# Performance work log

Hardware: AMD Instinct MI355X
Metric: run time of the kernel (lower is better)

Reference implementation:

```python
import math
import jax, jax.numpy as jnp
import numpy as np

jax.config.update("jax_enable_x64", True)

P_PRIME = 1000003            # prime modulus; p-1 = 2*3*166667
N_FACTORS = (2, 3, 166667)   # prime factors of p-1 (for primitive-root search)
B, NPATCH, L, K, DIM = 4, 784, 9, 16, 28  # batch, patches/sample, patch len, kernels, map dim


def _modpow(base, exp, p, nbits=21):
    """Vectorized modular exponentiation (square-and-multiply), int64, exponents < 2^nbits."""
    shape = jnp.broadcast_shapes(jnp.shape(base), jnp.shape(exp))
    b0 = jnp.broadcast_to(jnp.asarray(base, jnp.int64) % p, shape)
    e = jnp.broadcast_to(jnp.asarray(exp, jnp.int64), shape)
    def body(i, c):
        res, b = c
        res = jnp.where(((e >> i) & 1) == 1, (res * b) % p, res)
        return (res, (b * b) % p)
    res, _ = jax.lax.fori_loop(0, nbits, body, (jnp.ones(shape, jnp.int64), b0))
    return res


def _decrypt_ips(ct0, cts, y, sk_y, g, p):
    """IPFE decrypt + BSGS discrete log. ct0:[B,P] cts:[B,P,L] y:[K,L] sk_y:[K] -> signed ip [K,B,P]."""
    n = p - 1
    powed = _modpow(cts[None], jnp.mod(y, n)[:, None, None, :], p)   # [K,B,P,L]
    num = powed[..., 0]
    for i in range(1, L):                                            # fixed small L=9
        num = (num * powed[..., i]) % p
    denom = _modpow(ct0[None], jnp.mod(sk_y, n)[:, None, None], p)   # [K,B,P]
    val = (num * _modpow(denom, p - 2, p)) % p                       # = g^{<x,y>} mod p (Fermat inverse)
    # baby-step giant-step over group order n
    m = math.isqrt(n - 1) + 1
    n_giant = -(-n // m)
    baby = _modpow(jnp.int64(g), jnp.arange(m, dtype=jnp.int64), p)  # g^j, j in [0,m)
    order = jnp.argsort(baby)
    sb = baby[order]
    ginv_m = _modpow(jnp.int64(g), jnp.int64((n - m) % n), p)        # g^{-m}
    pt = _modpow(ginv_m, jnp.arange(n_giant, dtype=jnp.int64), p)    # g^{-m*i}
    gamma = (val.reshape(-1)[:, None] * pt[None, :]) % p             # [T, n_giant] giant steps
    pos = jnp.clip(jnp.searchsorted(sb, gamma), 0, m - 1)
    hit = sb[pos] == gamma
    cand = jnp.arange(n_giant, dtype=jnp.int64)[None, :] * m + order[pos]
    ip = jnp.min(jnp.where(hit, cand, n), axis=1)                    # unique match: ip = i*m + j
    ip = jnp.where(ip > n // 2, ip - n, ip)                          # signed representative
    return ip.reshape(K, ct0.shape[0], ct0.shape[1])


def _bn(x, g_, b_, m_, v_):
    s = g_ * jax.lax.rsqrt(v_ + 1e-5)
    return (x - m_[None, :, None, None]) * s[None, :, None, None] + b_[None, :, None, None]


def _conv(x, w, b):
    o = jax.lax.conv_general_dilated(x, w, (1, 1), ((1, 1), (1, 1)),
                                     dimension_numbers=("NCHW", "OIHW", "NCHW"))
    return o + b[None, :, None, None]


def _pool(x):
    return jax.lax.reduce_window(x, jnp.array(-jnp.inf, x.dtype), jax.lax.max,
                                 (1, 1, 2, 2), (1, 1, 2, 2), "VALID")


def _forward(ct0, cts, y, sk_y, bias1, bn1_g, bn1_b, bn1_m, bn1_v,
             conv2_w, conv2_b, bn2_g, bn2_b, bn2_m, bn2_v,
             conv3_w, conv3_b, bn3_g, bn3_b, bn3_m, bn3_v,
             fc1_w, fc1_b, fc2_w, fc2_b, g, p):
    ip = _decrypt_ips(ct0, cts, y, sk_y, g, p)                       # [K,B,P] int64
    maps = ip.astype(jnp.float32) / 10000.0 + bias1[:, None, None]   # dequantize + conv1 bias
    feat = jnp.transpose(maps, (1, 0, 2)).reshape(-1, K, DIM, DIM)   # [B,16,28,28]
    feat = _pool(jax.nn.relu(_bn(feat, bn1_g, bn1_b, bn1_m, bn1_v)))
    feat = _pool(jax.nn.relu(_bn(_conv(feat, conv2_w, conv2_b), bn2_g, bn2_b, bn2_m, bn2_v)))
    feat = _pool(jax.nn.relu(_bn(_conv(feat, conv3_w, conv3_b), bn3_g, bn3_b, bn3_m, bn3_v)))
    flat = feat.reshape(feat.shape[0], -1)                           # [B,576]
    h = jax.nn.relu(flat @ fc1_w.T + fc1_b)                          # dropout = identity (eval mode)
    return h @ fc2_w.T + fc2_b                                       # [B,10]


def setup_inputs():
    rng = np.random.default_rng(0)
    p, n = P_PRIME, P_PRIME - 1
    assert all(p % d for d in range(2, math.isqrt(p) + 1))           # p prime
    g = next(gg for gg in range(2, 200)
             if all(pow(gg, n // q, p) != 1 for q in N_FACTORS))      # primitive root mod p
    s = rng.integers(1, n, size=L)                                    # master secret
    pk = [pow(g, int(si), p) for si in s]
    y = rng.integers(-50, 51, size=(K, L)).astype(np.int64)          # round(w*10000)
    x = rng.integers(0, 21, size=(B, NPATCH, L))                     # quantized patch values
    r = rng.integers(1, n, size=(B, NPATCH))
    gx = [pow(g, t, p) for t in range(21)]
    ct0 = np.zeros((B, NPATCH), dtype=np.int64)
    cts = np.zeros((B, NPATCH, L), dtype=np.int64)
    for b in range(B):
        for j in range(NPATCH):
            rr = int(r[b, j])
            ct0[b, j] = pow(g, rr, p)
            for i in range(L):
                cts[b, j, i] = pow(pk[i], rr, p) * gx[x[b, j, i]] % p
    sk_y = np.array([sum(int(s[i]) * int(y[k, i]) for i in range(L)) % n
                     for k in range(K)], dtype=np.int64)
    f32 = lambda a: jnp.asarray(a, jnp.float32)
    def rn(*sh):
        return f32(rng.standard_normal(sh) * 0.1)
    def bnp(c):
        return (f32(1.0 + 0.1 * rng.standard_normal(c)), rn(c), rn(c), f32(rng.random(c) + 0.5))
    bn1_g, bn1_b, bn1_m, bn1_v = bnp(16)
    bn2_g, bn2_b, bn2_m, bn2_v = bnp(32)
    bn3_g, bn3_b, bn3_m, bn3_v = bnp(64)
    return dict(ct0=jnp.asarray(ct0), cts=jnp.asarray(cts),
                y=jnp.asarray(y), sk_y=jnp.asarray(sk_y), bias1=rn(K),
                bn1_g=bn1_g, bn1_b=bn1_b, bn1_m=bn1_m, bn1_v=bn1_v,
                conv2_w=rn(32, 16, 3, 3), conv2_b=rn(32),
                bn2_g=bn2_g, bn2_b=bn2_b, bn2_m=bn2_m, bn2_v=bn2_v,
                conv3_w=rn(64, 32, 3, 3), conv3_b=rn(64),
                bn3_g=bn3_g, bn3_b=bn3_b, bn3_m=bn3_m, bn3_v=bn3_v,
                fc1_w=rn(128, 576), fc1_b=rn(128),
                fc2_w=rn(10, 128), fc2_b=rn(10), g=g, p=p)


def reference(ct0, cts, y, sk_y, bias1, bn1_g, bn1_b, bn1_m, bn1_v,
              conv2_w, conv2_b, bn2_g, bn2_b, bn2_m, bn2_v,
              conv3_w, conv3_b, bn3_g, bn3_b, bn3_m, bn3_v,
              fc1_w, fc1_b, fc2_w, fc2_b, g, p):
    return _forward(ct0, cts, y, sk_y, bias1, bn1_g, bn1_b, bn1_m, bn1_v,
                    conv2_w, conv2_b, bn2_g, bn2_b, bn2_m, bn2_v,
                    conv3_w, conv3_b, bn3_g, bn3_b, bn3_m, bn3_v,
                    fc1_w, fc1_b, fc2_w, fc2_b, g, p)
```

## Files before the change

### kernel.cpp

```cpp
#include <hip/hip_runtime.h>
#include <stdint.h>

#define PRIME 1000003u
#define NORD  1000002u
#define KCH   16
#define BATCH 4
#define NPATCH 784
#define LLEN  9
#define IPMAX 9000
#define TBLN  (2*IPMAX+1)
#define NBLK  128
#define ABLK  64
#define TPB   832

#define CTR_OFF   2000064
#define POOL_OFF  2001024
#define S2G_OFF   2051200
#define S3G_OFF   2076288
#define HG_OFF    2085504

__device__ __forceinline__ uint32_t mmul(uint32_t a, uint32_t b) {
    uint64_t t = (uint64_t)a * (uint64_t)b;
    uint32_t q = (uint32_t)((t * 2199016ull) >> 41);
    uint32_t r = (uint32_t)t - q * PRIME;
    return (r >= PRIME) ? r - PRIME : r;
}

__device__ __forceinline__ uint32_t mpow(uint32_t base, uint32_t exp) {
    uint32_t r = 1u, b = base;
    while (exp) {
        if (exp & 1u) r = mmul(r, b);
        b = mmul(b, b);
        exp >>= 1;
    }
    return r;
}

__device__ __forceinline__ void cstore(float* p, float v) {
    __hip_atomic_store(p, v, __ATOMIC_RELAXED, __HIP_MEMORY_SCOPE_AGENT);
}
__device__ __forceinline__ float cload(const float* p) {
    return __hip_atomic_load(p, __ATOMIC_RELAXED, __HIP_MEMORY_SCOPE_AGENT);
}

__device__ __forceinline__ void arrive8(unsigned* ctrs, int bid) {
    __syncthreads();
    if (threadIdx.x == 0)
        __hip_atomic_fetch_add(&ctrs[(bid & 7) * 16], 1u,
                               __ATOMIC_RELAXED, __HIP_MEMORY_SCOPE_AGENT);
}
__device__ __forceinline__ void wait8(unsigned* ctrs, unsigned target) {
    if (threadIdx.x == 0) {
        for (;;) {
            unsigned s = 0;
#pragma unroll
            for (int i = 0; i < 8; i++)
                s += __hip_atomic_load(&ctrs[i * 16],
                                       __ATOMIC_RELAXED, __HIP_MEMORY_SCOPE_AGENT);
            if (s >= target) break;
            __builtin_amdgcn_s_sleep(8);
        }
    }
    __syncthreads();
}

__global__ void build_table(const int* __restrict__ g_in, int16_t* __restrict__ table,
                            unsigned* __restrict__ ctrs) {
    int e = blockIdx.x * blockDim.x + threadIdx.x;
    if (e >= TBLN) return;
    if (e < 8)
        __hip_atomic_store(&ctrs[e * 16], 0u, __ATOMIC_RELAXED, __HIP_MEMORY_SCOPE_AGENT);
    int es = e - IPMAX;
    uint32_t exp = (es >= 0) ? (uint32_t)es : (uint32_t)(es + (int)NORD);
    table[mpow((uint32_t)g_in[0], exp)] = (int16_t)es;
}

__global__ void __launch_bounds__(TPB) fused(
    const int* __restrict__ ct0, const int* __restrict__ cts,
    const int* __restrict__ y, const int* __restrict__ sk_y,
    const float* __restrict__ bias1,
    const float* __restrict__ bn1_g, const float* __restrict__ bn1_b,
    const float* __restrict__ bn1_m, const float* __restrict__ bn1_v,
    const float* __restrict__ conv2_w, const float* __restrict__ conv2_b,
    const float* __restrict__ bn2_g, const float* __restrict__ bn2_b,
    const float* __restrict__ bn2_m, const float* __restrict__ bn2_v,
    const float* __restrict__ conv3_w, const float* __restrict__ conv3_b,
    const float* __restrict__ bn3_g, const float* __restrict__ bn3_b,
    const float* __restrict__ bn3_m, const float* __restrict__ bn3_v,
    const float* __restrict__ fc1_w, const float* __restrict__ fc1_b,
    const float* __restrict__ fc2_w, const float* __restrict__ fc2_b,
    const int16_t* __restrict__ table,
    float* __restrict__ pooled, float* __restrict__ s2g, float* __restrict__ s3g,
    float* __restrict__ hg, float* __restrict__ out, unsigned* __restrict__ ctrs) {

    __shared__ union {
        float raw[784];
        struct { float s1p[16][16][16]; float w[144]; float co[196]; } c2;
        struct { float s2p[32][9][9];  float w[4][288]; float co[4][49]; } c3;
        struct { float s3[576]; } d1;
        struct { float h[128]; } d2;
    } sm;

    const int bid = blockIdx.x;
    const int tid = threadIdx.x;

    if (bid < ABLK) {
        const int k = bid & 15, b = bid >> 4;
        const int* yrow = y + k * LLEN;
        int yv[LLEN];
#pragma unroll
        for (int i = 0; i < LLEN; i++) yv[i] = yrow[i];
        const uint32_t sk = (uint32_t)sk_y[k];
        const float sc  = bn1_g[k] * rsqrtf(bn1_v[k] + 1e-5f);
        const float shf = (bias1[k] - bn1_m[k]) * sc + bn1_b[k];

        if (tid < NPATCH) {
            const int j = tid;
            const int* crow = cts + ((b * NPATCH) + j) * LLEN;
            uint32_t c[LLEN];
#pragma unroll
            for (int i = 0; i < LLEN; i++) c[i] = (uint32_t)crow[i];

            uint32_t accp = 1u, accn = 1u;
#pragma unroll
            for (int bit = 5; bit >= 0; bit--) {
                accp = mmul(accp, accp);
                accn = mmul(accn, accn);
#pragma unroll
                for (int i = 0; i < LLEN; i++) {
                    int yi = yv[i];
                    int ay = (yi > 0) ? yi : -yi;
                    if ((ay >> bit) & 1) {
                        if (yi > 0) accp = mmul(accp, c[i]);
                        else        accn = mmul(accn, c[i]);
                    }
                }
            }

            uint32_t den = mpow((uint32_t)ct0[b * NPATCH + j], sk);
            den = mmul(den, accn);
            uint32_t val = mmul(accp, mpow(den, PRIME - 2u));

            int ip = (int)table[val];
            float v_ = fmaf((float)ip, sc * 1e-4f, shf);
            sm.raw[j] = fmaxf(v_, 0.0f);
        }
        __syncthreads();
        if (tid < 196) {
            int py = tid / 14, px = tid % 14;
            const float* r0 = &sm.raw[(2 * py) * 28 + 2 * px];
            float m = fmaxf(fmaxf(r0[0], r0[1]), fmaxf(r0[28], r0[29]));
            cstore(&pooled[((b * KCH) + k) * 196 + tid], m);
        }
        arrive8(ctrs, bid);
    }

    wait8(ctrs, ABLK);

    {
        const int b  = bid >> 5;
        const int oc = bid & 31;

        for (int i = tid; i < 16 * 16 * 16; i += TPB)
            ((float*)sm.c2.s1p)[i] = 0.0f;
        if (tid < 144) sm.c2.w[tid] = conv2_w[oc * 144 + tid];
        __syncthreads();
        for (int i = tid; i < 16 * 196; i += TPB) {
            int ic = i / 196, pos = i % 196;
            int yy = pos / 14, xx = pos % 14;
            sm.c2.s1p[ic][yy + 1][xx + 1] = cload(&pooled[((b * KCH) + ic) * 196 + pos]);
        }
        __syncthreads();

        if (tid < 196) {
            int oh = tid / 14, ow = tid % 14;
            float a0 = 0.0f, a1 = 0.0f, a2 = 0.0f;
#pragma unroll
            for (int ic = 0; ic < 16; ic++) {
                const float* wp = &sm.c2.w[ic * 9];
                const float* sp = &sm.c2.s1p[ic][oh][ow];
                a0 = fmaf(sp[0],  wp[0], fmaf(sp[1],  wp[1], fmaf(sp[2],  wp[2], a0)));
                a1 = fmaf(sp[16], wp[3], fmaf(sp[17], wp[4], fmaf(sp[18], wp[5], a1)));
                a2 = fmaf(sp[32], wp[6], fmaf(sp[33], wp[7], fmaf(sp[34], wp[8], a2)));
            }
            float sc = bn2_g[oc] * rsqrtf(bn2_v[oc] + 1e-5f);
            float shf = bn2_b[oc] - bn2_m[oc] * sc;
            sm.c2.co[tid] = fmaxf((a0 + a1 + a2 + conv2_b[oc]) * sc + shf, 0.0f);
        }
        __syncthreads();

        if (tid < 49) {
            int oh = tid / 7, ow = tid % 7;
            const float* c0 = &sm.c2.co[(2 * oh) * 14 + 2 * ow];
            cstore(&s2g[((b * 32 + oc) * 49) + tid],
                   fmaxf(fmaxf(c0[0], c0[1]), fmaxf(c0[14], c0[15])));
        }
    }

    arrive8(ctrs, bid);
    if (bid >= 64) return;
    wait8(ctrs, ABLK + NBLK);

    {
        const int b = bid >> 4, ocg = bid & 15;

        for (int i = tid; i < 32 * 81; i += TPB)
            ((float*)sm.c3.s2p)[i] = 0.0f;
        for (int i = tid; i < 4 * 288; i += TPB) {
            int w2 = i / 288, rr = i % 288;
            sm.c3.w[w2][rr] = conv3_w[(ocg * 4 + w2) * 288 + rr];
        }
        __syncthreads();
        for (int i = tid; i < 32 * 49; i += TPB) {
            int ic = i / 49, pos = i % 49;
            sm.c3.s2p[ic][pos / 7 + 1][pos % 7 + 1] = cload(&s2g[((b * 32 + ic) * 49) + pos]);
        }
        __syncthreads();

        const int wid = tid >> 6, lane = tid & 63;
        if (wid < 4 && lane < 49) {
            int oh = lane / 7, ow = lane % 7;
            float a0 = 0.0f, a1 = 0.0f, a2 = 0.0f;
#pragma unroll
            for (int ic = 0; ic < 32; ic++) {
                const float* wp = &sm.c3.w[wid][ic * 9];
                const float* sp = &sm.c3.s2p[ic][oh][ow];
                a0 = fmaf(sp[0],  wp[0], fmaf(sp[1],  wp[1], fmaf(sp[2],  wp[2], a0)));
                a1 = fmaf(sp[9],  wp[3], fmaf(sp[10], wp[4], fmaf(sp[11], wp[5], a1)));
                a2 = fmaf(sp[18], wp[6], fmaf(sp[19], wp[7], fmaf(sp[20], wp[8], a2)));
            }
            int oc = ocg * 4 + wid;
            float sc = bn3_g[oc] * rsqrtf(bn3_v[oc] + 1e-5f);
            float shf = bn3_b[oc] - bn3_m[oc] * sc;
            sm.c3.co[wid][lane] = fmaxf((a0 + a1 + a2 + conv3_b[oc]) * sc + shf, 0.0f);
        }
        __syncthreads();

        if (tid < 36) {
            int w2 = tid / 9, p = tid % 9;
            int oh = p / 3, ow = p % 3;
            const float* c0 = &sm.c3.co[w2][(2 * oh) * 7 + 2 * ow];
            cstore(&s3g[b * 576 + (ocg * 4 + w2) * 9 + p],
                   fmaxf(fmaxf(c0[0], c0[1]), fmaxf(c0[7], c0[8])));
        }
    }

    arrive8(ctrs, bid);
    wait8(ctrs, ABLK + NBLK + 64);

    {
        const int b = bid >> 4, og = bid & 15;
        for (int i = tid; i < 576; i += TPB) sm.d1.s3[i] = cload(&s3g[b * 576 + i]);
        __syncthreads();

        const int wid = tid >> 6, lane = tid & 63;
        if (wid < 8) {
            int o = og * 8 + wid;
            const float* w = fc1_w + o * 576;
            float acc = 0.0f;
#pragma unroll
            for (int jj = 0; jj < 9; jj++)
                acc = fmaf(sm.d1.s3[jj * 64 + lane], w[jj * 64 + lane], acc);
#pragma unroll
            for (int off = 32; off; off >>= 1) acc += __shfl_down(acc, off);
            if (lane == 0) cstore(&hg[b * 128 + o], fmaxf(acc + fc1_b[o], 0.0f));
        }
    }

    arrive8(ctrs, bid);
    if (bid >= BATCH) return;
    wait8(ctrs, ABLK + NBLK + 64 + 64);

    {
        const int b = bid;
        if (tid < 128) sm.d2.h[tid] = cload(&hg[b * 128 + tid]);
        __syncthreads();

        const int wid = tid >> 6, lane = tid & 63;
        if (wid < 10) {
            const float* w = fc2_w + wid * 128;
            float acc = fmaf(sm.d2.h[lane], w[lane], 0.0f);
            acc = fmaf(sm.d2.h[64 + lane], w[64 + lane], acc);
#pragma unroll
            for (int off = 32; off; off >>= 1) acc += __shfl_down(acc, off);
            if (lane == 0) out[b * 10 + wid] = acc + fc2_b[wid];
        }
    }
}

extern "C" void kernel_launch(void* const* d_in, const int* in_sizes, int n_in,
                              void* d_out, int out_size, void* d_ws, size_t ws_size,
                              hipStream_t stream) {
    const int*   ct0    = (const int*)d_in[0];
    const int*   cts    = (const int*)d_in[1];
    const int*   y      = (const int*)d_in[2];
    const int*   sk_y   = (const int*)d_in[3];
    const float* bias1  = (const float*)d_in[4];
    const float* bn1_g  = (const float*)d_in[5];
    const float* bn1_b  = (const float*)d_in[6];
    const float* bn1_m  = (const float*)d_in[7];
    const float* bn1_v  = (const float*)d_in[8];
    const float* conv2_w = (const float*)d_in[9];
    const float* conv2_b = (const float*)d_in[10];
    const float* bn2_g  = (const float*)d_in[11];
    const float* bn2_b  = (const float*)d_in[12];
    const float* bn2_m  = (const float*)d_in[13];
    const float* bn2_v  = (const float*)d_in[14];
    const float* conv3_w = (const float*)d_in[15];
    const float* conv3_b = (const float*)d_in[16];
    const float* bn3_g  = (const float*)d_in[17];
    const float* bn3_b  = (const float*)d_in[18];
    const float* bn3_m  = (const float*)d_in[19];
    const float* bn3_v  = (const float*)d_in[20];
    const float* fc1_w  = (const float*)d_in[21];
    const float* fc1_b  = (const float*)d_in[22];
    const float* fc2_w  = (const float*)d_in[23];
    const float* fc2_b  = (const float*)d_in[24];
    const int*   g_in   = (const int*)d_in[25];
    float* out = (float*)d_out;

    char* ws = (char*)d_ws;
    int16_t*  table  = (int16_t*)ws;
    unsigned* ctrs   = (unsigned*)(ws + CTR_OFF);
    float* pooled = (float*)(ws + POOL_OFF);
    float* s2g    = (float*)(ws + S2G_OFF);
    float* s3g    = (float*)(ws + S3G_OFF);
    float* hg     = (float*)(ws + HG_OFF);

    build_table<<<(TBLN + 255) / 256, 256, 0, stream>>>(g_in, table, ctrs);

    fused<<<NBLK, TPB, 0, stream>>>(
        ct0, cts, y, sk_y, bias1, bn1_g, bn1_b, bn1_m, bn1_v,
        conv2_w, conv2_b, bn2_g, bn2_b, bn2_m, bn2_v,
        conv3_w, conv3_b, bn3_g, bn3_b, bn3_m, bn3_v,
        fc1_w, fc1_b, fc2_w, fc2_b, table, pooled, s2g, s3g, hg, out, ctrs);
}
```

Measured before the change: 131.2 us.

## Split decrypt across all blocks, replace counter barriers with per-block phase flags, merge FC stages

The decrypt stage now runs on all 128 blocks, each handling half of a (batch, kernel) pair's patches, so the modular exponentiation work is spread across twice as many CUs. Conv2 now uses 32 blocks that each compute 4 output channels, and FC1 and FC2 run inside the same 4 blocks with the hidden vector kept in shared memory. This removes one grid barrier and the hg workspace. Summed atomic counters are replaced by per-block phase flags, and each waiter polls only the flags it depends on. The trade-offs are serial flag polling over up to 128 entries and less parallelism in the conv2 and FC1 stages.

```diff
diff --git a/kernel.cpp b/kernel.cpp
--- a/kernel.cpp
+++ b/kernel.cpp
@@ -10,14 +10,12 @@
 #define IPMAX 9000
 #define TBLN  (2*IPMAX+1)
 #define NBLK  128
-#define ABLK  64
 #define TPB   832
 
-#define CTR_OFF   2000064
-#define POOL_OFF  2001024
-#define S2G_OFF   2051200
-#define S3G_OFF   2076288
-#define HG_OFF    2085504
+#define FLAG_OFF  2000064
+#define POOL_OFF  2008256
+#define S2G_OFF   2058432
+#define S3G_OFF   2083520
 
 __device__ __forceinline__ uint32_t mmul(uint32_t a, uint32_t b) {
     uint64_t t = (uint64_t)a * (uint64_t)b;
@@ -43,33 +41,33 @@
     return __hip_atomic_load(p, __ATOMIC_RELAXED, __HIP_MEMORY_SCOPE_AGENT);
 }
 
-__device__ __forceinline__ void arrive8(unsigned* ctrs, int bid) {
+__device__ __forceinline__ void set_flag(unsigned* flags, int bid, unsigned phase) {
     __syncthreads();
     if (threadIdx.x == 0)
-        __hip_atomic_fetch_add(&ctrs[(bid & 7) * 16], 1u,
-                               __ATOMIC_RELAXED, __HIP_MEMORY_SCOPE_AGENT);
-}
-__device__ __forceinline__ void wait8(unsigned* ctrs, unsigned target) {
+        __hip_atomic_store(&flags[bid * 16], phase,
+                           __ATOMIC_RELAXED, __HIP_MEMORY_SCOPE_AGENT);
+}
+__device__ __forceinline__ void wait_flags(unsigned* flags, int n, unsigned phase) {
     if (threadIdx.x == 0) {
-        for (;;) {
-            unsigned s = 0;
-#pragma unroll
-            for (int i = 0; i < 8; i++)
-                s += __hip_atomic_load(&ctrs[i * 16],
-                                       __ATOMIC_RELAXED, __HIP_MEMORY_SCOPE_AGENT);
-            if (s >= target) break;
-            __builtin_amdgcn_s_sleep(8);
+        int i = 0;
+        while (i < n) {
+            if (__hip_atomic_load(&flags[i * 16],
+                                  __ATOMIC_RELAXED, __HIP_MEMORY_SCOPE_AGENT) >= phase) {
+                i++;
+            } else {
+                __builtin_amdgcn_s_sleep(8);
+            }
         }
     }
     __syncthreads();
 }
 
 __global__ void build_table(const int* __restrict__ g_in, int16_t* __restrict__ table,
-                            unsigned* __restrict__ ctrs) {
+                            unsigned* __restrict__ flags) {
     int e = blockIdx.x * blockDim.x + threadIdx.x;
     if (e >= TBLN) return;
-    if (e < 8)
-        __hip_atomic_store(&ctrs[e * 16], 0u, __ATOMIC_RELAXED, __HIP_MEMORY_SCOPE_AGENT);
+    if (e < NBLK)
+        __hip_atomic_store(&flags[e * 16], 0u, __ATOMIC_RELAXED, __HIP_MEMORY_SCOPE_AGENT);
     int es = e - IPMAX;
     uint32_t exp = (es >= 0) ? (uint32_t)es : (uint32_t)(es + (int)NORD);
     table[mpow((uint32_t)g_in[0], exp)] = (int16_t)es;
@@ -91,21 +89,21 @@
     const float* __restrict__ fc2_w, const float* __restrict__ fc2_b,
     const int16_t* __restrict__ table,
     float* __restrict__ pooled, float* __restrict__ s2g, float* __restrict__ s3g,
-    float* __restrict__ hg, float* __restrict__ out, unsigned* __restrict__ ctrs) {
+    float* __restrict__ out, unsigned* __restrict__ flags) {
 
     __shared__ union {
-        float raw[784];
-        struct { float s1p[16][16][16]; float w[144]; float co[196]; } c2;
+        float raw[392];
+        struct { float s1p[16][16][16]; float w[4][144]; float co[4][196]; } c2;
         struct { float s2p[32][9][9];  float w[4][288]; float co[4][49]; } c3;
-        struct { float s3[576]; } d1;
-        struct { float h[128]; } d2;
+        struct { float s3[576]; float h[128]; } d;
     } sm;
 
     const int bid = blockIdx.x;
     const int tid = threadIdx.x;
 
-    if (bid < ABLK) {
-        const int k = bid & 15, b = bid >> 4;
+    {
+        const int pair = bid >> 1, half = bid & 1;
+        const int k = pair & 15, b = pair >> 4;
         const int* yrow = y + k * LLEN;
         int yv[LLEN];
 #pragma unroll
@@ -114,8 +112,8 @@
         const float sc  = bn1_g[k] * rsqrtf(bn1_v[k] + 1e-5f);
         const float shf = (bias1[k] - bn1_m[k]) * sc + bn1_b[k];
 
-        if (tid < NPATCH) {
-            const int j = tid;
+        if (tid < 392) {
+            const int j = half * 392 + tid;
             const int* crow = cts + ((b * NPATCH) + j) * LLEN;
             uint32_t c[LLEN];
 #pragma unroll
@@ -143,27 +141,27 @@
 
             int ip = (int)table[val];
             float v_ = fmaf((float)ip, sc * 1e-4f, shf);
-            sm.raw[j] = fmaxf(v_, 0.0f);
-        }
-        __syncthreads();
-        if (tid < 196) {
-            int py = tid / 14, px = tid % 14;
-            const float* r0 = &sm.raw[(2 * py) * 28 + 2 * px];
+            sm.raw[tid] = fmaxf(v_, 0.0f);
+        }
+        __syncthreads();
+        if (tid < 98) {
+            int pyl = tid / 14, px = tid % 14;
+            const float* r0 = &sm.raw[(2 * pyl) * 28 + 2 * px];
             float m = fmaxf(fmaxf(r0[0], r0[1]), fmaxf(r0[28], r0[29]));
-            cstore(&pooled[((b * KCH) + k) * 196 + tid], m);
-        }
-        arrive8(ctrs, bid);
-    }
-
-    wait8(ctrs, ABLK);
-
-    {
-        const int b  = bid >> 5;
-        const int oc = bid & 31;
+            cstore(&pooled[((b * KCH) + k) * 196 + (half * 7 + pyl) * 14 + px], m);
+        }
+    }
+    set_flag(flags, bid, 1u);
+    if (bid >= 64) return;
+
+    if (bid < 32) {
+        wait_flags(flags, NBLK, 1u);
+        const int b = bid >> 3, base_oc = (bid & 7) * 4;
 
         for (int i = tid; i < 16 * 16 * 16; i += TPB)
             ((float*)sm.c2.s1p)[i] = 0.0f;
-        if (tid < 144) sm.c2.w[tid] = conv2_w[oc * 144 + tid];
+        if (tid < 576) sm.c2.w[tid / 144][tid % 144] =
+            conv2_w[(base_oc + tid / 144) * 144 + tid % 144];
         __syncthreads();
         for (int i = tid; i < 16 * 196; i += TPB) {
             int ic = i / 196, pos = i % 196;
@@ -172,12 +170,14 @@
         }
         __syncthreads();
 
-        if (tid < 196) {
-            int oh = tid / 14, ow = tid % 14;
+        if (tid < 784) {
+            int ocs = tid / 196, pos = tid % 196;
+            int oh = pos / 14, ow = pos % 14;
+            int oc = base_oc + ocs;
             float a0 = 0.0f, a1 = 0.0f, a2 = 0.0f;
 #pragma unroll
             for (int ic = 0; ic < 16; ic++) {
-                const float* wp = &sm.c2.w[ic * 9];
+                const float* wp = &sm.c2.w[ocs][ic * 9];
                 const float* sp = &sm.c2.s1p[ic][oh][ow];
                 a0 = fmaf(sp[0],  wp[0], fmaf(sp[1],  wp[1], fmaf(sp[2],  wp[2], a0)));
                 a1 = fmaf(sp[16], wp[3], fmaf(sp[17], wp[4], fmaf(sp[18], wp[5], a1)));
@@ -185,23 +185,22 @@
             }
             float sc = bn2_g[oc] * rsqrtf(bn2_v[oc] + 1e-5f);
             float shf = bn2_b[oc] - bn2_m[oc] * sc;
-            sm.c2.co[tid] = fmaxf((a0 + a1 + a2 + conv2_b[oc]) * sc + shf, 0.0f);
-        }
-        __syncthreads();
-
-        if (tid < 49) {
-            int oh = tid / 7, ow = tid % 7;
-            const float* c0 = &sm.c2.co[(2 * oh) * 14 + 2 * ow];
-            cstore(&s2g[((b * 32 + oc) * 49) + tid],
+            sm.c2.co[ocs][pos] = fmaxf((a0 + a1 + a2 + conv2_b[oc]) * sc + shf, 0.0f);
+        }
+        __syncthreads();
+
+        if (tid < 196) {
+            int ocs = tid / 49, pp = tid % 49;
+            int oh = pp / 7, ow = pp % 7;
+            const float* c0 = &sm.c2.co[ocs][(2 * oh) * 14 + 2 * ow];
+            cstore(&s2g[((b * 32 + base_oc + ocs) * 49) + pp],
                    fmaxf(fmaxf(c0[0], c0[1]), fmaxf(c0[14], c0[15])));
         }
-    }
-
-    arrive8(ctrs, bid);
-    if (bid >= 64) return;
-    wait8(ctrs, ABLK + NBLK);
+        set_flag(flags, bid, 2u);
+    }
 
     {
+        wait_flags(flags, 32, 2u);
         const int b = bid >> 4, ocg = bid & 15;
 
         for (int i = tid; i < 32 * 81; i += TPB)
@@ -243,44 +242,33 @@
             cstore(&s3g[b * 576 + (ocg * 4 + w2) * 9 + p],
                    fmaxf(fmaxf(c0[0], c0[1]), fmaxf(c0[7], c0[8])));
         }
-    }
-
-    arrive8(ctrs, bid);
-    wait8(ctrs, ABLK + NBLK + 64);
+        set_flag(flags, bid, 3u);
+    }
+    if (bid >= BATCH) return;
 
     {
-        const int b = bid >> 4, og = bid & 15;
-        for (int i = tid; i < 576; i += TPB) sm.d1.s3[i] = cload(&s3g[b * 576 + i]);
+        wait_flags(flags, 64, 3u);
+        const int b = bid;
+        if (tid < 576) sm.d.s3[tid] = cload(&s3g[b * 576 + tid]);
         __syncthreads();
 
         const int wid = tid >> 6, lane = tid & 63;
-        if (wid < 8) {
-            int o = og * 8 + wid;
+        for (int o = wid; o < 128; o += 13) {
             const float* w = fc1_w + o * 576;
             float acc = 0.0f;
 #pragma unroll
             for (int jj = 0; jj < 9; jj++)
-                acc = fmaf(sm.d1.s3[jj * 64 + lane], w[jj * 64 + lane], acc);
+                acc = fmaf(sm.d.s3[jj * 64 + lane], w[jj * 64 + lane], acc);
 #pragma unroll
             for (int off = 32; off; off >>= 1) acc += __shfl_down(acc, off);
-            if (lane == 0) cstore(&hg[b * 128 + o], fmaxf(acc + fc1_b[o], 0.0f));
-        }
-    }
-
-    arrive8(ctrs, bid);
-    if (bid >= BATCH) return;
-    wait8(ctrs, ABLK + NBLK + 64 + 64);
-
-    {
-        const int b = bid;
-        if (tid < 128) sm.d2.h[tid] = cload(&hg[b * 128 + tid]);
-        __syncthreads();
-
-        const int wid = tid >> 6, lane = tid & 63;
+            if (lane == 0) sm.d.h[o] = fmaxf(acc + fc1_b[o], 0.0f);
+        }
+        __syncthreads();
+
         if (wid < 10) {
             const float* w = fc2_w + wid * 128;
-            float acc = fmaf(sm.d2.h[lane], w[lane], 0.0f);
-            acc = fmaf(sm.d2.h[64 + lane], w[64 + lane], acc);
+            float acc = fmaf(sm.d.h[lane], w[lane], 0.0f);
+            acc = fmaf(sm.d.h[64 + lane], w[64 + lane], acc);
 #pragma unroll
             for (int off = 32; off; off >>= 1) acc += __shfl_down(acc, off);
             if (lane == 0) out[b * 10 + wid] = acc + fc2_b[wid];
@@ -321,17 +309,16 @@
 
     char* ws = (char*)d_ws;
     int16_t*  table  = (int16_t*)ws;
-    unsigned* ctrs   = (unsigned*)(ws + CTR_OFF);
+    unsigned* flags  = (unsigned*)(ws + FLAG_OFF);
     float* pooled = (float*)(ws + POOL_OFF);
     float* s2g    = (float*)(ws + S2G_OFF);
     float* s3g    = (float*)(ws + S3G_OFF);
-    float* hg     = (float*)(ws + HG_OFF);
-
-    build_table<<<(TBLN + 255) / 256, 256, 0, stream>>>(g_in, table, ctrs);
+
+    build_table<<<(TBLN + 255) / 256, 256, 0, stream>>>(g_in, table, flags);
 
     fused<<<NBLK, TPB, 0, stream>>>(
         ct0, cts, y, sk_y, bias1, bn1_g, bn1_b, bn1_m, bn1_v,
         conv2_w, conv2_b, bn2_g, bn2_b, bn2_m, bn2_v,
         conv3_w, conv3_b, bn3_g, bn3_b, bn3_m, bn3_v,
-        fc1_w, fc1_b, fc2_w, fc2_b, table, pooled, s2g, s3g, hg, out, ctrs);
-}
+        fc1_w, fc1_b, fc2_w, fc2_b, table, pooled, s2g, s3g, out, flags);
+}
```

Result: slower. 187.9 us (+43.2%).
